# Performance work log

Measured on AMD Instinct MI355X. Metric: run time of the kernel, lower is better.

The kernel has to match this reference:

```python
import jax, jax.numpy as jnp
import numpy as np

N = 100000
E = 1000000
D = 32          # numerical_dim
HID = 64        # hidden_dim
OUT = 1         # output_dim
REL = 4 * D     # relation feature dim
EPS = 1e-8


def setup_inputs() -> dict:
    key = jax.random.key(0)
    k_x, k_e, k_w1, k_b1, k_w2, k_b2 = jax.random.split(key, 6)
    x = jax.random.uniform(k_x, (N, D), dtype=jnp.float32)
    edge_index = jax.random.randint(k_e, (2, E), 0, N, dtype=jnp.int64)
    # Linear params (PyTorch convention: W [out, in], y = x @ W.T + b)
    lim1 = 1.0 / np.sqrt(REL)
    W1 = jax.random.uniform(k_w1, (HID, REL), minval=-lim1, maxval=lim1, dtype=jnp.float32)
    b1 = jax.random.uniform(k_b1, (HID,), minval=-lim1, maxval=lim1, dtype=jnp.float32)
    lim2 = 1.0 / np.sqrt(HID)
    W2 = jax.random.uniform(k_w2, (OUT, HID), minval=-lim2, maxval=lim2, dtype=jnp.float32)
    b2 = jax.random.uniform(k_b2, (OUT,), minval=-lim2, maxval=lim2, dtype=jnp.float32)
    return {"x": x, "edge_index": edge_index, "W1": W1, "b1": b1, "W2": W2, "b2": b2}


def _relation_features(x_i, x_j):
    ratio = x_i / (x_j + EPS)
    log_ratio = jnp.log(x_i + EPS) - jnp.log(x_j + EPS)
    abs_diff = jnp.abs(x_i - x_j)
    rel_diff = abs_diff / (jnp.maximum(x_i, x_j) + EPS)
    return jnp.concatenate([ratio, log_ratio, abs_diff, rel_diff], axis=-1)  # [E, 4D]


def reference(x, edge_index, W1, b1, W2, b2):
    src, dst = edge_index[0], edge_index[1]
    x_i = x[src]                      # [E, D] gather source node feats
    x_j = x[dst]                      # [E, D] gather target node feats
    rel = _relation_features(x_i, x_j)  # [E, 4D]
    h = jax.nn.relu(rel @ W1.T + b1)    # [E, HID]
    edge_bias = (h @ W2.T + b2).squeeze(-1)  # [E]
    return edge_bias
```

## Files before the change

kernel.cpp:

```cpp
#include <hip/hip_runtime.h>


#define DD    32
#define HID   64
#define RELF  128
#define EPSF  1e-8f
#define LXLO  -18.420681f
#define LXSC  13.843137f
#define LXIV  0.07223796f
#define MSC   3.0517578125e-05f

typedef short  bf16x8 __attribute__((ext_vector_type(8)));
typedef float  f32x4  __attribute__((ext_vector_type(4)));

union U8 { unsigned u[4]; bf16x8 v; uint4 q4; };
union Q  { uint4 v; unsigned u[4]; float f[4]; };

static __device__ __forceinline__ unsigned pk_tr(float lo, float hi) {
    return __builtin_amdgcn_perm(__builtin_bit_cast(unsigned, hi),
                                 __builtin_bit_cast(unsigned, lo), 0x07060302u);
}
static __device__ __forceinline__ unsigned rne_bits(float f) {
    unsigned u = __builtin_bit_cast(unsigned, f);
    return u + 0x7fffu + ((u >> 16) & 1u);
}
static __device__ __forceinline__ unsigned pk_rne(float lo, float hi) {
    return __builtin_amdgcn_perm(rne_bits(hi), rne_bits(lo), 0x07060302u);
}
static __device__ __forceinline__ float hi_f32(float f) {
    return __builtin_bit_cast(float, __builtin_bit_cast(unsigned, f) & 0xffff0000u);
}
static __device__ __forceinline__ float ubyte(unsigned w, int b) {
    return (float)((w >> (8 * b)) & 0xffu);
}
static __device__ __forceinline__ unsigned q8(float v) {
    int u = (int)(v + 0.5f);
    return (unsigned)(u > 255 ? 255 : (u < 0 ? 0 : u));
}
template <int CTRL>
static __device__ __forceinline__ float dpp_ror_add(float pp) {
    int s = __builtin_bit_cast(int, pp);
    int t = __builtin_amdgcn_update_dpp(0, s, CTRL, 0xf, 0xf, true);
    return pp + __builtin_bit_cast(float, t);
}

__global__ __launch_bounds__(256)
void prep_pack(const float* __restrict__ x, uint4* __restrict__ rec, int nchunk)
{
    int i = blockIdx.x * blockDim.x + threadIdx.x;
    if (i >= nchunk) return;
    const float4* xp = (const float4*)(x + (size_t)i * 8);
    float4 v0 = xp[0], v1 = xp[1];
    float xv[8] = {v0.x, v0.y, v0.z, v0.w, v1.x, v1.y, v1.z, v1.w};

    unsigned xh[4];
    #pragma unroll
    for (int p = 0; p < 4; ++p) xh[p] = pk_tr(xv[2*p], xv[2*p+1]);

    unsigned xl[2] = {0u, 0u}, lu[2] = {0u, 0u};
    #pragma unroll
    for (int e = 0; e < 8; ++e) {
        float a  = xv[e];
        float ah = hi_f32(a);
        float f  = 0.f;
        if (ah > 0.f)
            f = (a * __builtin_amdgcn_rcpf(ah) - 1.f) * 32768.f;
        xl[e >> 2] |= q8(f) << (8 * (e & 3));
        float lxe = __logf(a + EPSF);
        lu[e >> 2] |= q8((lxe - LXLO) * LXSC) << (8 * (e & 3));
    }

    uint4 r0; r0.x = xh[0]; r0.y = xh[1]; r0.z = xh[2]; r0.w = xh[3];
    uint4 r1; r1.x = xl[0]; r1.y = xl[1]; r1.z = lu[0]; r1.w = lu[1];
    rec[2 * i]     = r0;
    rec[2 * i + 1] = r1;
}

template <int PACK>
__global__ __launch_bounds__(256, 4)
void edge_bias_mfma(const float* __restrict__ x,
                    const int*   __restrict__ ei,
                    const float* __restrict__ W1,
                    const float* __restrict__ b1,
                    const float* __restrict__ W2,
                    const float* __restrict__ b2,
                    const uint4* __restrict__ rec,
                    float* __restrict__ out,
                    int E)
{
    const int lane = threadIdx.x & 63;
    const int wv   = threadIdx.x >> 6;
    const int wave = (blockIdx.x * blockDim.x + threadIdx.x) >> 6;
    const int nwv  = (gridDim.x * blockDim.x) >> 6;
    const int c = lane & 15;
    const int q = lane >> 4;

    __shared__ uint4 sW[20 * 64];
    for (int s = wv; s < 5; s += 4) {
        #pragma unroll
        for (int nt = 0; nt < 4; ++nt) {
            const float* wr = W1 + (nt * 16 + c) * RELF + q * 8;
            U8 t;
            if (s == 0) {
                #pragma unroll
                for (int p = 0; p < 4; ++p)
                    t.u[p] = pk_tr(wr[2*p], wr[2*p+1]);
            } else if (s == 1) {
                #pragma unroll
                for (int p = 0; p < 4; ++p) {
                    float w0 = wr[2*p], w1 = wr[2*p+1];
                    t.u[p] = pk_rne(w0 - hi_f32(w0), w1 - hi_f32(w1));
                }
            } else {
                const int base = (s == 2) ? 32 : (s == 3) ? 64 : 96;
                #pragma unroll
                for (int p = 0; p < 4; ++p)
                    t.u[p] = pk_rne(wr[base + 2*p], wr[base + 2*p + 1]);
            }
            sW[(s * 4 + nt) * 64 + lane] = t.q4;
        }
    }
    __syncthreads();

    float b1v[4], w2v[4];
    #pragma unroll
    for (int nt = 0; nt < 4; ++nt) {
        b1v[nt] = b1[nt * 16 + c];
        w2v[nt] = W2[nt * 16 + c];
    }
    const float b2s = b2[0];

    const int ntiles = (E + 15) >> 4;
    int t = wave;
    if (t >= ntiles) return;

    auto ldidx = [&](int tt_, int& s, int& d) {
        if (tt_ >= ntiles) tt_ = t;
        int em = (tt_ << 4) + c; if (em > E - 1) em = E - 1;
        s = ei[em]; d = ei[E + em];
    };
    auto gather = [&](int s, int d, Q& hi_, Q& mi_, Q& hj_, Q& mj_) {
        if constexpr (PACK) {
            const uint4* pi = rec + (size_t)s * 8 + q * 2;
            const uint4* pj = rec + (size_t)d * 8 + q * 2;
            hi_.v = pi[0]; mi_.v = pi[1];
            hj_.v = pj[0]; mj_.v = pj[1];
        } else {
            const uint4* pi = (const uint4*)(x + (size_t)s * DD + q * 8);
            const uint4* pj = (const uint4*)(x + (size_t)d * DD + q * 8);
            hi_.v = pi[0]; mi_.v = pi[1];
            hj_.v = pj[0]; mj_.v = pj[1];
        }
    };
    auto decode = [&](const Q& h, const Q& m, float* xv, bf16x8& lfrag) {
        #pragma unroll
        for (int p = 0; p < 4; ++p) {
            float lo = __builtin_bit_cast(float, h.u[p] << 16);
            float hi = __builtin_bit_cast(float, h.u[p] & 0xffff0000u);
            unsigned xb = (p < 2) ? m.u[0] : m.u[1];
            float m0 = ubyte(xb, (2 * p) & 3);
            float m1 = ubyte(xb, (2 * p + 1) & 3);
            xv[2 * p]     = fmaf(lo * MSC, m0, lo);
            xv[2 * p + 1] = fmaf(hi * MSC, m1, hi);
        }
        U8 L;
        #pragma unroll
        for (int p = 0; p < 4; ++p) {
            unsigned lb = (p < 2) ? m.u[2] : m.u[3];
            float l0 = fmaf(ubyte(lb, (2 * p) & 3),     LXIV, LXLO);
            float l1 = fmaf(ubyte(lb, (2 * p + 1) & 3), LXIV, LXLO);
            L.u[p] = pk_tr(l0, l1);
        }
        lfrag = L.v;
    };

    auto compute = [&](int tc, const Q& hI, const Q& mI, const Q& hJ, const Q& mJ) {
        float xiv[8], xjv[8];
        bf16x8 aLi, aLj;
        if constexpr (PACK) {
            decode(hI, mI, xiv, aLi);
            decode(hJ, mJ, xjv, aLj);
        } else {
            #pragma unroll
            for (int p = 0; p < 4; ++p) { xiv[p] = hI.f[p]; xiv[4 + p] = mI.f[p]; }
            #pragma unroll
            for (int p = 0; p < 4; ++p) { xjv[p] = hJ.f[p]; xjv[4 + p] = mJ.f[p]; }
            U8 ti, tj;
            #pragma unroll
            for (int p = 0; p < 4; ++p) {
                ti.u[p] = pk_rne(__logf(xiv[2*p] + EPSF), __logf(xiv[2*p+1] + EPSF));
                tj.u[p] = pk_rne(__logf(xjv[2*p] + EPSF), __logf(xjv[2*p+1] + EPSF));
            }
            aLi = ti.v; aLj = tj.v;
        }
        U8 nj; nj.v = aLj;
        #pragma unroll
        for (int p = 0; p < 4; ++p) nj.u[p] ^= 0x80008000u;

        U8 R, Rl, Aa, Dd;
        #pragma unroll
        for (int p = 0; p < 4; ++p) {
            float a0 = xiv[2*p], a1 = xiv[2*p+1];
            float c0 = xjv[2*p], c1 = xjv[2*p+1];
            float r0 = a0 * __builtin_amdgcn_rcpf(c0 + EPSF);
            float r1 = a1 * __builtin_amdgcn_rcpf(c1 + EPSF);
            float d0 = fabsf(a0 - c0), d1 = fabsf(a1 - c1);
            float g0 = d0 * __builtin_amdgcn_rcpf(fmaxf(a0, c0) + EPSF);
            float g1 = d1 * __builtin_amdgcn_rcpf(fmaxf(a1, c1) + EPSF);
            R.u[p]  = pk_tr(r0, r1);
            Rl.u[p] = pk_tr(r0 - hi_f32(r0), r1 - hi_f32(r1));
            Aa.u[p] = pk_tr(d0, d1);
            Dd.u[p] = pk_tr(g0, g1);
        }

        int off = lane;
        asm volatile("" : "+v"(off));
        auto ldfrag = [&](int s, int nt) {
            U8 w; w.q4 = sW[(s * 4 + nt) * 64 + off];
            return w.v;
        };

        f32x4 acc[4];
        #pragma unroll
        for (int nt = 0; nt < 4; ++nt) {
            acc[nt][0] = b1v[nt]; acc[nt][1] = b1v[nt];
            acc[nt][2] = b1v[nt]; acc[nt][3] = b1v[nt];
        }
        #pragma unroll
        for (int nt = 0; nt < 4; ++nt) {
            bf16x8 fW0h = ldfrag(0, nt);
            bf16x8 fW0l = ldfrag(1, nt);
            bf16x8 fWL  = ldfrag(2, nt);
            bf16x8 fWA  = ldfrag(3, nt);
            bf16x8 fWD  = ldfrag(4, nt);
            acc[nt] = __builtin_amdgcn_mfma_f32_16x16x32_bf16(R.v,  fW0h, acc[nt], 0, 0, 0);
            acc[nt] = __builtin_amdgcn_mfma_f32_16x16x32_bf16(Rl.v, fW0h, acc[nt], 0, 0, 0);
            acc[nt] = __builtin_amdgcn_mfma_f32_16x16x32_bf16(R.v,  fW0l, acc[nt], 0, 0, 0);
            acc[nt] = __builtin_amdgcn_mfma_f32_16x16x32_bf16(aLi,  fWL,  acc[nt], 0, 0, 0);
            acc[nt] = __builtin_amdgcn_mfma_f32_16x16x32_bf16(nj.v, fWL,  acc[nt], 0, 0, 0);
            acc[nt] = __builtin_amdgcn_mfma_f32_16x16x32_bf16(Aa.v, fWA,  acc[nt], 0, 0, 0);
            acc[nt] = __builtin_amdgcn_mfma_f32_16x16x32_bf16(Dd.v, fWD,  acc[nt], 0, 0, 0);
        }

        float p4[4];
        #pragma unroll
        for (int r = 0; r < 4; ++r) {
            float pp = 0.f;
            #pragma unroll
            for (int nt = 0; nt < 4; ++nt)
                pp = fmaf(fmaxf(acc[nt][r], 0.f), w2v[nt], pp);
            pp = dpp_ror_add<0x121>(pp);
            pp = dpp_ror_add<0x122>(pp);
            pp = dpp_ror_add<0x124>(pp);
            pp = dpp_ror_add<0x128>(pp);
            p4[r] = pp;
        }
        if (c < 4) {
            const int e = (tc << 4) + q * 4 + c;
            if (e < E) {
                float v = (c == 0) ? p4[0] : (c == 1) ? p4[1] : (c == 2) ? p4[2] : p4[3];
                out[e] = v + b2s;
            }
        }
    };

    Q hA, mA, hJA, mJA;
    Q hB, mB, hJB, mJB;
    int sC, dC;

    { int s, d; ldidx(t,        s, d); gather(s, d, hA, mA, hJA, mJA); }
    { int s, d; ldidx(t + nwv,  s, d); gather(s, d, hB, mB, hJB, mJB); }
    ldidx(t + 2 * nwv, sC, dC);

    for (;;) {
        compute(t, hA, mA, hJA, mJA);
        gather(sC, dC, hA, mA, hJA, mJA);
        ldidx(t + 3 * nwv, sC, dC);
        t += nwv; if (t >= ntiles) break;

        compute(t, hB, mB, hJB, mJB);
        gather(sC, dC, hB, mB, hJB, mJB);
        ldidx(t + 3 * nwv, sC, dC);
        t += nwv; if (t >= ntiles) break;
    }
}

extern "C" void kernel_launch(void* const* d_in, const int* in_sizes, int n_in,
                              void* d_out, int out_size, void* d_ws, size_t ws_size,
                              hipStream_t stream)
{
    const float* x   = (const float*)d_in[0];
    const int*   ei  = (const int*)  d_in[1];
    const float* W1  = (const float*)d_in[2];
    const float* b1  = (const float*)d_in[3];
    const float* W2  = (const float*)d_in[4];
    const float* b2  = (const float*)d_in[5];
    float* out = (float*)d_out;

    const int E  = out_size;
    const int Nd = in_sizes[0];
    uint4* rec = (uint4*)d_ws;

    const bool pack = ws_size >= (size_t)Nd * 4 && (Nd % 8) == 0;
    if (pack) {
        const int nchunk = Nd / 8;
        prep_pack<<<(nchunk + 255) / 256, 256, 0, stream>>>(x, rec, nchunk);
        edge_bias_mfma<1><<<2048, 256, 0, stream>>>(x, ei, W1, b1, W2, b2, rec, out, E);
    } else {
        edge_bias_mfma<0><<<2048, 256, 0, stream>>>(x, ei, W1, b1, W2, b2, rec, out, E);
    }
}
```

Before: 131.6 us.

## Switch edge MLP to 32x32x16 MFMA tiles and drop software prefetch pipeline

Changes the per-wave tile from 16 to 32 edges and replaces the 16x16x32 bf16 MFMAs with 32x32x16 ones over two K-slices. The weight fragments in LDS are relaid out to match, and the output reduction uses an extra DPP step plus a lane-select tree. The explicit double-buffered gather/index prefetch loop is removed in favour of a simple grid-stride loop, and the grid shrinks to 1954 blocks. The aim is fewer MFMA issues and better operand reuse per edge, at the cost of losing the explicit latency hiding for the random gathers.

```diff
diff --git a/kernel.cpp b/kernel.cpp
--- a/kernel.cpp
+++ b/kernel.cpp
@@ -12,6 +12,7 @@
 
 typedef short  bf16x8 __attribute__((ext_vector_type(8)));
 typedef float  f32x4  __attribute__((ext_vector_type(4)));
+typedef float  f32x16 __attribute__((ext_vector_type(16)));
 
 union U8 { unsigned u[4]; bf16x8 v; uint4 q4; };
 union Q  { uint4 v; unsigned u[4]; float f[4]; };
@@ -92,72 +93,46 @@
     const int wv   = threadIdx.x >> 6;
     const int wave = (blockIdx.x * blockDim.x + threadIdx.x) >> 6;
     const int nwv  = (gridDim.x * blockDim.x) >> 6;
-    const int c = lane & 15;
-    const int q = lane >> 4;
+    const int r = lane & 31;
+    const int h = lane >> 5;
 
     __shared__ uint4 sW[20 * 64];
-    for (int s = wv; s < 5; s += 4) {
-        #pragma unroll
-        for (int nt = 0; nt < 4; ++nt) {
-            const float* wr = W1 + (nt * 16 + c) * RELF + q * 8;
-            U8 t;
-            if (s == 0) {
-                #pragma unroll
-                for (int p = 0; p < 4; ++p)
-                    t.u[p] = pk_tr(wr[2*p], wr[2*p+1]);
-            } else if (s == 1) {
-                #pragma unroll
-                for (int p = 0; p < 4; ++p) {
-                    float w0 = wr[2*p], w1 = wr[2*p+1];
-                    t.u[p] = pk_rne(w0 - hi_f32(w0), w1 - hi_f32(w1));
-                }
-            } else {
-                const int base = (s == 2) ? 32 : (s == 3) ? 64 : 96;
-                #pragma unroll
-                for (int p = 0; p < 4; ++p)
-                    t.u[p] = pk_rne(wr[base + 2*p], wr[base + 2*p + 1]);
+    for (int f = wv; f < 20; f += 4) {
+        const int set = f >> 2, ct = (f >> 1) & 1, sl = f & 1;
+        const int fb  = (set <= 1) ? 0 : (set - 1) * 32;
+        const float* wr = W1 + (ct * 32 + r) * RELF + fb + sl * 16 + h * 8;
+        U8 tw;
+        if (set == 0) {
+            #pragma unroll
+            for (int p = 0; p < 4; ++p) tw.u[p] = pk_tr(wr[2*p], wr[2*p+1]);
+        } else if (set == 1) {
+            #pragma unroll
+            for (int p = 0; p < 4; ++p) {
+                float w0 = wr[2*p], w1 = wr[2*p+1];
+                tw.u[p] = pk_rne(w0 - hi_f32(w0), w1 - hi_f32(w1));
             }
-            sW[(s * 4 + nt) * 64 + lane] = t.q4;
-        }
+        } else {
+            #pragma unroll
+            for (int p = 0; p < 4; ++p) tw.u[p] = pk_rne(wr[2*p], wr[2*p+1]);
+        }
+        sW[f * 64 + lane] = tw.q4;
     }
     __syncthreads();
 
-    float b1v[4], w2v[4];
+    float b1v[2], w2v[2];
     #pragma unroll
-    for (int nt = 0; nt < 4; ++nt) {
-        b1v[nt] = b1[nt * 16 + c];
-        w2v[nt] = W2[nt * 16 + c];
+    for (int ct = 0; ct < 2; ++ct) {
+        b1v[ct] = b1[ct * 32 + r];
+        w2v[ct] = W2[ct * 32 + r];
     }
     const float b2s = b2[0];
 
-    const int ntiles = (E + 15) >> 4;
-    int t = wave;
-    if (t >= ntiles) return;
-
-    auto ldidx = [&](int tt_, int& s, int& d) {
-        if (tt_ >= ntiles) tt_ = t;
-        int em = (tt_ << 4) + c; if (em > E - 1) em = E - 1;
-        s = ei[em]; d = ei[E + em];
-    };
-    auto gather = [&](int s, int d, Q& hi_, Q& mi_, Q& hj_, Q& mj_) {
-        if constexpr (PACK) {
-            const uint4* pi = rec + (size_t)s * 8 + q * 2;
-            const uint4* pj = rec + (size_t)d * 8 + q * 2;
-            hi_.v = pi[0]; mi_.v = pi[1];
-            hj_.v = pj[0]; mj_.v = pj[1];
-        } else {
-            const uint4* pi = (const uint4*)(x + (size_t)s * DD + q * 8);
-            const uint4* pj = (const uint4*)(x + (size_t)d * DD + q * 8);
-            hi_.v = pi[0]; mi_.v = pi[1];
-            hj_.v = pj[0]; mj_.v = pj[1];
-        }
-    };
-    auto decode = [&](const Q& h, const Q& m, float* xv, bf16x8& lfrag) {
+    auto decode = [&](const Q& hq, const Q& mq, float* xv, bf16x8& lfrag) {
         #pragma unroll
         for (int p = 0; p < 4; ++p) {
-            float lo = __builtin_bit_cast(float, h.u[p] << 16);
-            float hi = __builtin_bit_cast(float, h.u[p] & 0xffff0000u);
-            unsigned xb = (p < 2) ? m.u[0] : m.u[1];
+            float lo = __builtin_bit_cast(float, hq.u[p] << 16);
+            float hi = __builtin_bit_cast(float, hq.u[p] & 0xffff0000u);
+            unsigned xb = (p < 2) ? mq.u[0] : mq.u[1];
             float m0 = ubyte(xb, (2 * p) & 3);
             float m1 = ubyte(xb, (2 * p + 1) & 3);
             xv[2 * p]     = fmaf(lo * MSC, m0, lo);
@@ -166,7 +141,7 @@
         U8 L;
         #pragma unroll
         for (int p = 0; p < 4; ++p) {
-            unsigned lb = (p < 2) ? m.u[2] : m.u[3];
+            unsigned lb = (p < 2) ? mq.u[2] : mq.u[3];
             float l0 = fmaf(ubyte(lb, (2 * p) & 3),     LXIV, LXLO);
             float l1 = fmaf(ubyte(lb, (2 * p + 1) & 3), LXIV, LXLO);
             L.u[p] = pk_tr(l0, l1);
@@ -174,114 +149,135 @@
         lfrag = L.v;
     };
 
-    auto compute = [&](int tc, const Q& hI, const Q& mI, const Q& hJ, const Q& mJ) {
-        float xiv[8], xjv[8];
-        bf16x8 aLi, aLj;
+    const int ntiles = (E + 31) >> 5;
+    for (int t = wave; t < ntiles; t += nwv) {
+        int em = (t << 5) + r; if (em > E - 1) em = E - 1;
+        const int sn = ei[em], dn = ei[E + em];
+
+        Q hi0, mi0, hi1, mi1, hj0, mj0, hj1, mj1;
         if constexpr (PACK) {
-            decode(hI, mI, xiv, aLi);
-            decode(hJ, mJ, xjv, aLj);
+            const uint4* pi = rec + (size_t)sn * 8 + (h << 1);
+            const uint4* pj = rec + (size_t)dn * 8 + (h << 1);
+            hi0.v = pi[0]; mi0.v = pi[1]; hi1.v = pi[4]; mi1.v = pi[5];
+            hj0.v = pj[0]; mj0.v = pj[1]; hj1.v = pj[4]; mj1.v = pj[5];
         } else {
-            #pragma unroll
-            for (int p = 0; p < 4; ++p) { xiv[p] = hI.f[p]; xiv[4 + p] = mI.f[p]; }
-            #pragma unroll
-            for (int p = 0; p < 4; ++p) { xjv[p] = hJ.f[p]; xjv[4 + p] = mJ.f[p]; }
-            U8 ti, tj;
-            #pragma unroll
-            for (int p = 0; p < 4; ++p) {
-                ti.u[p] = pk_rne(__logf(xiv[2*p] + EPSF), __logf(xiv[2*p+1] + EPSF));
-                tj.u[p] = pk_rne(__logf(xjv[2*p] + EPSF), __logf(xjv[2*p+1] + EPSF));
-            }
-            aLi = ti.v; aLj = tj.v;
-        }
-        U8 nj; nj.v = aLj;
-        #pragma unroll
-        for (int p = 0; p < 4; ++p) nj.u[p] ^= 0x80008000u;
-
-        U8 R, Rl, Aa, Dd;
-        #pragma unroll
-        for (int p = 0; p < 4; ++p) {
-            float a0 = xiv[2*p], a1 = xiv[2*p+1];
-            float c0 = xjv[2*p], c1 = xjv[2*p+1];
-            float r0 = a0 * __builtin_amdgcn_rcpf(c0 + EPSF);
-            float r1 = a1 * __builtin_amdgcn_rcpf(c1 + EPSF);
-            float d0 = fabsf(a0 - c0), d1 = fabsf(a1 - c1);
-            float g0 = d0 * __builtin_amdgcn_rcpf(fmaxf(a0, c0) + EPSF);
-            float g1 = d1 * __builtin_amdgcn_rcpf(fmaxf(a1, c1) + EPSF);
-            R.u[p]  = pk_tr(r0, r1);
-            Rl.u[p] = pk_tr(r0 - hi_f32(r0), r1 - hi_f32(r1));
-            Aa.u[p] = pk_tr(d0, d1);
-            Dd.u[p] = pk_tr(g0, g1);
+            const uint4* pi = (const uint4*)(x + (size_t)sn * DD + h * 8);
+            const uint4* pj = (const uint4*)(x + (size_t)dn * DD + h * 8);
+            hi0.v = pi[0]; mi0.v = pi[1]; hi1.v = pi[4]; mi1.v = pi[5];
+            hj0.v = pj[0]; mj0.v = pj[1]; hj1.v = pj[4]; mj1.v = pj[5];
         }
 
         int off = lane;
         asm volatile("" : "+v"(off));
-        auto ldfrag = [&](int s, int nt) {
-            U8 w; w.q4 = sW[(s * 4 + nt) * 64 + off];
+        auto ldfrag = [&](int set, int ct, int sl) {
+            U8 w; w.q4 = sW[(set * 4 + ct * 2 + sl) * 64 + off];
             return w.v;
         };
 
-        f32x4 acc[4];
-        #pragma unroll
-        for (int nt = 0; nt < 4; ++nt) {
-            acc[nt][0] = b1v[nt]; acc[nt][1] = b1v[nt];
-            acc[nt][2] = b1v[nt]; acc[nt][3] = b1v[nt];
-        }
-        #pragma unroll
-        for (int nt = 0; nt < 4; ++nt) {
-            bf16x8 fW0h = ldfrag(0, nt);
-            bf16x8 fW0l = ldfrag(1, nt);
-            bf16x8 fWL  = ldfrag(2, nt);
-            bf16x8 fWA  = ldfrag(3, nt);
-            bf16x8 fWD  = ldfrag(4, nt);
-            acc[nt] = __builtin_amdgcn_mfma_f32_16x16x32_bf16(R.v,  fW0h, acc[nt], 0, 0, 0);
-            acc[nt] = __builtin_amdgcn_mfma_f32_16x16x32_bf16(Rl.v, fW0h, acc[nt], 0, 0, 0);
-            acc[nt] = __builtin_amdgcn_mfma_f32_16x16x32_bf16(R.v,  fW0l, acc[nt], 0, 0, 0);
-            acc[nt] = __builtin_amdgcn_mfma_f32_16x16x32_bf16(aLi,  fWL,  acc[nt], 0, 0, 0);
-            acc[nt] = __builtin_amdgcn_mfma_f32_16x16x32_bf16(nj.v, fWL,  acc[nt], 0, 0, 0);
-            acc[nt] = __builtin_amdgcn_mfma_f32_16x16x32_bf16(Aa.v, fWA,  acc[nt], 0, 0, 0);
-            acc[nt] = __builtin_amdgcn_mfma_f32_16x16x32_bf16(Dd.v, fWD,  acc[nt], 0, 0, 0);
-        }
-
-        float p4[4];
-        #pragma unroll
-        for (int r = 0; r < 4; ++r) {
-            float pp = 0.f;
-            #pragma unroll
-            for (int nt = 0; nt < 4; ++nt)
-                pp = fmaf(fmaxf(acc[nt][r], 0.f), w2v[nt], pp);
-            pp = dpp_ror_add<0x121>(pp);
-            pp = dpp_ror_add<0x122>(pp);
-            pp = dpp_ror_add<0x124>(pp);
-            pp = dpp_ror_add<0x128>(pp);
-            p4[r] = pp;
-        }
-        if (c < 4) {
-            const int e = (tc << 4) + q * 4 + c;
-            if (e < E) {
-                float v = (c == 0) ? p4[0] : (c == 1) ? p4[1] : (c == 2) ? p4[2] : p4[3];
-                out[e] = v + b2s;
+        f32x16 acc0, acc1;
+        #pragma unroll
+        for (int i = 0; i < 16; ++i) { acc0[i] = b1v[0]; acc1[i] = b1v[1]; }
+
+        #pragma unroll
+        for (int sl = 0; sl < 2; ++sl) {
+            const Q& hI = sl ? hi1 : hi0;  const Q& mI = sl ? mi1 : mi0;
+            const Q& hJ = sl ? hj1 : hj0;  const Q& mJ = sl ? mj1 : mj0;
+
+            float xiv[8], xjv[8];
+            bf16x8 aLi, aLj;
+            if constexpr (PACK) {
+                decode(hI, mI, xiv, aLi);
+                decode(hJ, mJ, xjv, aLj);
+            } else {
+                #pragma unroll
+                for (int p = 0; p < 4; ++p) {
+                    xiv[p] = hI.f[p]; xiv[4 + p] = mI.f[p];
+                    xjv[p] = hJ.f[p]; xjv[4 + p] = mJ.f[p];
+                }
+                U8 ti, tj;
+                #pragma unroll
+                for (int p = 0; p < 4; ++p) {
+                    ti.u[p] = pk_rne(__logf(xiv[2*p] + EPSF), __logf(xiv[2*p+1] + EPSF));
+                    tj.u[p] = pk_rne(__logf(xjv[2*p] + EPSF), __logf(xjv[2*p+1] + EPSF));
+                }
+                aLi = ti.v; aLj = tj.v;
             }
-        }
-    };
-
-    Q hA, mA, hJA, mJA;
-    Q hB, mB, hJB, mJB;
-    int sC, dC;
-
-    { int s, d; ldidx(t,        s, d); gather(s, d, hA, mA, hJA, mJA); }
-    { int s, d; ldidx(t + nwv,  s, d); gather(s, d, hB, mB, hJB, mJB); }
-    ldidx(t + 2 * nwv, sC, dC);
-
-    for (;;) {
-        compute(t, hA, mA, hJA, mJA);
-        gather(sC, dC, hA, mA, hJA, mJA);
-        ldidx(t + 3 * nwv, sC, dC);
-        t += nwv; if (t >= ntiles) break;
-
-        compute(t, hB, mB, hJB, mJB);
-        gather(sC, dC, hB, mB, hJB, mJB);
-        ldidx(t + 3 * nwv, sC, dC);
-        t += nwv; if (t >= ntiles) break;
+            U8 nj; nj.v = aLj;
+            #pragma unroll
+            for (int p = 0; p < 4; ++p) nj.u[p] ^= 0x80008000u;
+
+            U8 R, Rl, Aa, Dd;
+            #pragma unroll
+            for (int p = 0; p < 4; ++p) {
+                float a0 = xiv[2*p], a1 = xiv[2*p+1];
+                float c0 = xjv[2*p], c1 = xjv[2*p+1];
+                float r0 = a0 * __builtin_amdgcn_rcpf(c0 + EPSF);
+                float r1 = a1 * __builtin_amdgcn_rcpf(c1 + EPSF);
+                float d0 = fabsf(a0 - c0), d1 = fabsf(a1 - c1);
+                float g0 = d0 * __builtin_amdgcn_rcpf(fmaxf(a0, c0) + EPSF);
+                float g1 = d1 * __builtin_amdgcn_rcpf(fmaxf(a1, c1) + EPSF);
+                R.u[p]  = pk_tr(r0, r1);
+                Rl.u[p] = pk_tr(r0 - hi_f32(r0), r1 - hi_f32(r1));
+                Aa.u[p] = pk_tr(d0, d1);
+                Dd.u[p] = pk_tr(g0, g1);
+            }
+
+            #pragma unroll
+            for (int ct = 0; ct < 2; ++ct) {
+                bf16x8 fW0h = ldfrag(0, ct, sl);
+                bf16x8 fW0l = ldfrag(1, ct, sl);
+                bf16x8 fWL  = ldfrag(2, ct, sl);
+                bf16x8 fWA  = ldfrag(3, ct, sl);
+                bf16x8 fWD  = ldfrag(4, ct, sl);
+                if (ct == 0) {
+                    acc0 = __builtin_amdgcn_mfma_f32_32x32x16_bf16(R.v,  fW0h, acc0, 0, 0, 0);
+                    acc0 = __builtin_amdgcn_mfma_f32_32x32x16_bf16(Rl.v, fW0h, acc0, 0, 0, 0);
+                    acc0 = __builtin_amdgcn_mfma_f32_32x32x16_bf16(R.v,  fW0l, acc0, 0, 0, 0);
+                    acc0 = __builtin_amdgcn_mfma_f32_32x32x16_bf16(aLi,  fWL,  acc0, 0, 0, 0);
+                    acc0 = __builtin_amdgcn_mfma_f32_32x32x16_bf16(nj.v, fWL,  acc0, 0, 0, 0);
+                    acc0 = __builtin_amdgcn_mfma_f32_32x32x16_bf16(Aa.v, fWA,  acc0, 0, 0, 0);
+                    acc0 = __builtin_amdgcn_mfma_f32_32x32x16_bf16(Dd.v, fWD,  acc0, 0, 0, 0);
+                } else {
+                    acc1 = __builtin_amdgcn_mfma_f32_32x32x16_bf16(R.v,  fW0h, acc1, 0, 0, 0);
+                    acc1 = __builtin_amdgcn_mfma_f32_32x32x16_bf16(Rl.v, fW0h, acc1, 0, 0, 0);
+                    acc1 = __builtin_amdgcn_mfma_f32_32x32x16_bf16(R.v,  fW0l, acc1, 0, 0, 0);
+                    acc1 = __builtin_amdgcn_mfma_f32_32x32x16_bf16(aLi,  fWL,  acc1, 0, 0, 0);
+                    acc1 = __builtin_amdgcn_mfma_f32_32x32x16_bf16(nj.v, fWL,  acc1, 0, 0, 0);
+                    acc1 = __builtin_amdgcn_mfma_f32_32x32x16_bf16(Aa.v, fWA,  acc1, 0, 0, 0);
+                    acc1 = __builtin_amdgcn_mfma_f32_32x32x16_bf16(Dd.v, fWD,  acc1, 0, 0, 0);
+                }
+            }
+        }
+
+        float pp[16];
+        #pragma unroll
+        for (int g = 0; g < 16; ++g) {
+            float v0 = fmaxf(acc0[g], 0.f), v1 = fmaxf(acc1[g], 0.f);
+            pp[g] = fmaf(v0, w2v[0], v1 * w2v[1]);
+        }
+        #pragma unroll
+        for (int g = 0; g < 16; ++g) {
+            float s = pp[g];
+            s = dpp_ror_add<0x121>(s);
+            s = dpp_ror_add<0x122>(s);
+            s = dpp_ror_add<0x124>(s);
+            s = dpp_ror_add<0x128>(s);
+            s = dpp_ror_add<0x142>(s);
+            pp[g] = s;
+        }
+        if ((lane >> 4) & 1) {
+            const int l = lane & 15;
+            float q8a[8], q4a[4], q2a[2];
+            #pragma unroll
+            for (int i = 0; i < 8; ++i) q8a[i] = (l & 1) ? pp[2*i+1] : pp[2*i];
+            #pragma unroll
+            for (int i = 0; i < 4; ++i) q4a[i] = (l & 2) ? q8a[2*i+1] : q8a[2*i];
+            #pragma unroll
+            for (int i = 0; i < 2; ++i) q2a[i] = (l & 4) ? q4a[2*i+1] : q4a[2*i];
+            float v = (l & 8) ? q2a[1] : q2a[0];
+            const int e2 = (t << 5) + (l & 3) + ((l >> 2) << 3) + (h << 2);
+            if (e2 < E) out[e2] = v + b2s;
+        }
     }
 }
 
@@ -301,12 +297,14 @@
     const int Nd = in_sizes[0];
     uint4* rec = (uint4*)d_ws;
 
+    const int blocks = 1954;
+
     const bool pack = ws_size >= (size_t)Nd * 4 && (Nd % 8) == 0;
     if (pack) {
         const int nchunk = Nd / 8;
         prep_pack<<<(nchunk + 255) / 256, 256, 0, stream>>>(x, rec, nchunk);
-        edge_bias_mfma<1><<<2048, 256, 0, stream>>>(x, ei, W1, b1, W2, b2, rec, out, E);
+        edge_bias_mfma<1><<<blocks, 256, 0, stream>>>(x, ei, W1, b1, W2, b2, rec, out, E);
     } else {
-        edge_bias_mfma<0><<<2048, 256, 0, stream>>>(x, ei, W1, b1, W2, b2, rec, out, E);
-    }
-}
+        edge_bias_mfma<0><<<blocks, 256, 0, stream>>>(x, ei, W1, b1, W2, b2, rec, out, E);
+    }
+}
```

Result: slower. 239.7 us (+82.2%).

## Bucket-sort edges by source node before gathering to improve locality

Applied to the files above, without the earlier changes.

Adds a histogram/scan/scatter counting sort that groups edges by the high bits of their source index, then runs the MFMA edge kernel over the permuted edge list and scatters results back through the saved original index. The aim is better cache locality for the per-edge source-row gathers. In exchange it adds three extra launches, a serial single-block scan, extra index traffic and scattered output writes.

```diff
diff --git a/kernel.cpp b/kernel.cpp
--- a/kernel.cpp
+++ b/kernel.cpp
@@ -9,6 +9,9 @@
 #define LXSC  13.843137f
 #define LXIV  0.07223796f
 #define MSC   3.0517578125e-05f
+
+#define SB_NB 256
+#define SB_EB 8192
 
 typedef short  bf16x8 __attribute__((ext_vector_type(8)));
 typedef float  f32x4  __attribute__((ext_vector_type(4)));
@@ -76,10 +79,69 @@
     rec[2 * i + 1] = r1;
 }
 
-template <int PACK>
+__global__ __launch_bounds__(256)
+void sort_hist(const int* __restrict__ ei, unsigned* __restrict__ H,
+               int E, int shift)
+{
+    __shared__ unsigned lh[SB_NB];
+    const int tid = threadIdx.x, blk = blockIdx.x;
+    lh[tid] = 0u;
+    __syncthreads();
+    const int base = blk * SB_EB;
+    const int end  = (base + SB_EB < E) ? base + SB_EB : E;
+    for (int e = base + tid; e < end; e += 256)
+        atomicAdd(&lh[((unsigned)ei[e]) >> shift], 1u);
+    __syncthreads();
+    H[blk * SB_NB + tid] = lh[tid];
+}
+
+__global__ __launch_bounds__(256)
+void sort_scan(const unsigned* __restrict__ H, unsigned* __restrict__ Bk,
+               int nblk)
+{
+    __shared__ unsigned colsum[SB_NB];
+    __shared__ unsigned basebuf[SB_NB];
+    const int b = threadIdx.x;
+    unsigned s = 0;
+    for (int k = 0; k < nblk; ++k) s += H[k * SB_NB + b];
+    colsum[b] = s;
+    __syncthreads();
+    if (b == 0) {
+        unsigned run = 0;
+        for (int i = 0; i < SB_NB; ++i) { basebuf[i] = run; run += colsum[i]; }
+    }
+    __syncthreads();
+    unsigned run = basebuf[b];
+    for (int k = 0; k < nblk; ++k) {
+        Bk[k * SB_NB + b] = run;
+        run += H[k * SB_NB + b];
+    }
+}
+
+__global__ __launch_bounds__(256)
+void sort_scatter(const int* __restrict__ ei, const unsigned* __restrict__ Bk,
+                  int* __restrict__ ssrc, int* __restrict__ sdst,
+                  int* __restrict__ sidx, int E, int shift)
+{
+    __shared__ unsigned cur[SB_NB];
+    const int tid = threadIdx.x, blk = blockIdx.x;
+    cur[tid] = Bk[blk * SB_NB + tid];
+    __syncthreads();
+    const int base = blk * SB_EB;
+    const int end  = (base + SB_EB < E) ? base + SB_EB : E;
+    for (int e = base + tid; e < end; e += 256) {
+        int s = ei[e], d = ei[E + e];
+        unsigned pos = atomicAdd(&cur[((unsigned)s) >> shift], 1u);
+        ssrc[pos] = s; sdst[pos] = d; sidx[pos] = e;
+    }
+}
+
+template <int PACK, int SORTED>
 __global__ __launch_bounds__(256, 4)
 void edge_bias_mfma(const float* __restrict__ x,
-                    const int*   __restrict__ ei,
+                    const int*   __restrict__ psrc,
+                    const int*   __restrict__ pdst,
+                    const int*   __restrict__ pidx,
                     const float* __restrict__ W1,
                     const float* __restrict__ b1,
                     const float* __restrict__ W2,
@@ -137,7 +199,7 @@
     auto ldidx = [&](int tt_, int& s, int& d) {
         if (tt_ >= ntiles) tt_ = t;
         int em = (tt_ << 4) + c; if (em > E - 1) em = E - 1;
-        s = ei[em]; d = ei[E + em];
+        s = psrc[em]; d = pdst[em];
     };
     auto gather = [&](int s, int d, Q& hi_, Q& mi_, Q& hj_, Q& mj_) {
         if constexpr (PACK) {
@@ -259,7 +321,11 @@
             const int e = (tc << 4) + q * 4 + c;
             if (e < E) {
                 float v = (c == 0) ? p4[0] : (c == 1) ? p4[1] : (c == 2) ? p4[2] : p4[3];
-                out[e] = v + b2s;
+                if constexpr (SORTED) {
+                    out[pidx[e]] = v + b2s;
+                } else {
+                    out[e] = v + b2s;
+                }
             }
         }
     };
@@ -299,14 +365,41 @@
 
     const int E  = out_size;
     const int Nd = in_sizes[0];
-    uint4* rec = (uint4*)d_ws;
-
-    const bool pack = ws_size >= (size_t)Nd * 4 && (Nd % 8) == 0;
-    if (pack) {
+    const int N  = Nd / DD;
+
+    const size_t RB   = (size_t)Nd * 4;
+    const int    nblk = (E + SB_EB - 1) / SB_EB;
+    const size_t SORT = (size_t)E * 12 + (size_t)nblk * SB_NB * 8;
+
+    uint4*    rec  = (uint4*)d_ws;
+    char*     wb   = (char*)d_ws + RB;
+    int*      ssrc = (int*)wb;
+    int*      sdst = ssrc + E;
+    int*      sidx = sdst + E;
+    unsigned* H    = (unsigned*)(sidx + E);
+    unsigned* Bk   = H + (size_t)nblk * SB_NB;
+
+    const bool pack   = ws_size >= RB && (Nd % 8) == 0;
+    const bool sorted = pack && ws_size >= RB + SORT && E > 0;
+
+    int shift = 0;
+    while (((unsigned)(N - 1) >> shift) > 255u) ++shift;
+
+    if (sorted) {
         const int nchunk = Nd / 8;
         prep_pack<<<(nchunk + 255) / 256, 256, 0, stream>>>(x, rec, nchunk);
-        edge_bias_mfma<1><<<2048, 256, 0, stream>>>(x, ei, W1, b1, W2, b2, rec, out, E);
+        sort_hist<<<nblk, 256, 0, stream>>>(ei, H, E, shift);
+        sort_scan<<<1, 256, 0, stream>>>(H, Bk, nblk);
+        sort_scatter<<<nblk, 256, 0, stream>>>(ei, Bk, ssrc, sdst, sidx, E, shift);
+        edge_bias_mfma<1, 1><<<2048, 256, 0, stream>>>(
+            x, ssrc, sdst, sidx, W1, b1, W2, b2, rec, out, E);
+    } else if (pack) {
+        const int nchunk = Nd / 8;
+        prep_pack<<<(nchunk + 255) / 256, 256, 0, stream>>>(x, rec, nchunk);
+        edge_bias_mfma<1, 0><<<2048, 256, 0, stream>>>(
+            x, ei, ei + E, ei, W1, b1, W2, b2, rec, out, E);
     } else {
-        edge_bias_mfma<0><<<2048, 256, 0, stream>>>(x, ei, W1, b1, W2, b2, rec, out, E);
-    }
-}
+        edge_bias_mfma<0, 0><<<2048, 256, 0, stream>>>(
+            x, ei, ei + E, ei, W1, b1, W2, b2, rec, out, E);
+    }
+}
```

Measured after the change: 197.4 us. +50.0%, slower.

## Drop packed node-record precompute and gather raw fp32 features directly

Applied to the files above, without the earlier changes.

Removes the prep_pack pass that quantized node features into bf16-hi plus 8-bit mantissa and log codes. The edge kernel now always gathers raw fp32 rows and computes logs inline. This saves a kernel launch and the preprocessing traffic over all nodes. In exchange, each edge must recompute its log values and can no longer decode them from the precomputed codes. Gather bytes per edge are the same, since both paths read 32 bytes per quarter-row.

```diff
diff --git a/kernel.cpp b/kernel.cpp
--- a/kernel.cpp
+++ b/kernel.cpp
@@ -5,10 +5,6 @@
 #define HID   64
 #define RELF  128
 #define EPSF  1e-8f
-#define LXLO  -18.420681f
-#define LXSC  13.843137f
-#define LXIV  0.07223796f
-#define MSC   3.0517578125e-05f
 
 typedef short  bf16x8 __attribute__((ext_vector_type(8)));
 typedef float  f32x4  __attribute__((ext_vector_type(4)));
@@ -29,13 +25,6 @@
 }
 static __device__ __forceinline__ float hi_f32(float f) {
     return __builtin_bit_cast(float, __builtin_bit_cast(unsigned, f) & 0xffff0000u);
-}
-static __device__ __forceinline__ float ubyte(unsigned w, int b) {
-    return (float)((w >> (8 * b)) & 0xffu);
-}
-static __device__ __forceinline__ unsigned q8(float v) {
-    int u = (int)(v + 0.5f);
-    return (unsigned)(u > 255 ? 255 : (u < 0 ? 0 : u));
 }
 template <int CTRL>
 static __device__ __forceinline__ float dpp_ror_add(float pp) {
@@ -44,39 +33,6 @@
     return pp + __builtin_bit_cast(float, t);
 }
 
-__global__ __launch_bounds__(256)
-void prep_pack(const float* __restrict__ x, uint4* __restrict__ rec, int nchunk)
-{
-    int i = blockIdx.x * blockDim.x + threadIdx.x;
-    if (i >= nchunk) return;
-    const float4* xp = (const float4*)(x + (size_t)i * 8);
-    float4 v0 = xp[0], v1 = xp[1];
-    float xv[8] = {v0.x, v0.y, v0.z, v0.w, v1.x, v1.y, v1.z, v1.w};
-
-    unsigned xh[4];
-    #pragma unroll
-    for (int p = 0; p < 4; ++p) xh[p] = pk_tr(xv[2*p], xv[2*p+1]);
-
-    unsigned xl[2] = {0u, 0u}, lu[2] = {0u, 0u};
-    #pragma unroll
-    for (int e = 0; e < 8; ++e) {
-        float a  = xv[e];
-        float ah = hi_f32(a);
-        float f  = 0.f;
-        if (ah > 0.f)
-            f = (a * __builtin_amdgcn_rcpf(ah) - 1.f) * 32768.f;
-        xl[e >> 2] |= q8(f) << (8 * (e & 3));
-        float lxe = __logf(a + EPSF);
-        lu[e >> 2] |= q8((lxe - LXLO) * LXSC) << (8 * (e & 3));
-    }
-
-    uint4 r0; r0.x = xh[0]; r0.y = xh[1]; r0.z = xh[2]; r0.w = xh[3];
-    uint4 r1; r1.x = xl[0]; r1.y = xl[1]; r1.z = lu[0]; r1.w = lu[1];
-    rec[2 * i]     = r0;
-    rec[2 * i + 1] = r1;
-}
-
-template <int PACK>
 __global__ __launch_bounds__(256, 4)
 void edge_bias_mfma(const float* __restrict__ x,
                     const int*   __restrict__ ei,
@@ -84,7 +40,6 @@
                     const float* __restrict__ b1,
                     const float* __restrict__ W2,
                     const float* __restrict__ b2,
-                    const uint4* __restrict__ rec,
                     float* __restrict__ out,
                     int E)
 {
@@ -140,60 +95,27 @@
         s = ei[em]; d = ei[E + em];
     };
     auto gather = [&](int s, int d, Q& hi_, Q& mi_, Q& hj_, Q& mj_) {
-        if constexpr (PACK) {
-            const uint4* pi = rec + (size_t)s * 8 + q * 2;
-            const uint4* pj = rec + (size_t)d * 8 + q * 2;
-            hi_.v = pi[0]; mi_.v = pi[1];
-            hj_.v = pj[0]; mj_.v = pj[1];
-        } else {
-            const uint4* pi = (const uint4*)(x + (size_t)s * DD + q * 8);
-            const uint4* pj = (const uint4*)(x + (size_t)d * DD + q * 8);
-            hi_.v = pi[0]; mi_.v = pi[1];
-            hj_.v = pj[0]; mj_.v = pj[1];
-        }
-    };
-    auto decode = [&](const Q& h, const Q& m, float* xv, bf16x8& lfrag) {
-        #pragma unroll
-        for (int p = 0; p < 4; ++p) {
-            float lo = __builtin_bit_cast(float, h.u[p] << 16);
-            float hi = __builtin_bit_cast(float, h.u[p] & 0xffff0000u);
-            unsigned xb = (p < 2) ? m.u[0] : m.u[1];
-            float m0 = ubyte(xb, (2 * p) & 3);
-            float m1 = ubyte(xb, (2 * p + 1) & 3);
-            xv[2 * p]     = fmaf(lo * MSC, m0, lo);
-            xv[2 * p + 1] = fmaf(hi * MSC, m1, hi);
-        }
-        U8 L;
-        #pragma unroll
-        for (int p = 0; p < 4; ++p) {
-            unsigned lb = (p < 2) ? m.u[2] : m.u[3];
-            float l0 = fmaf(ubyte(lb, (2 * p) & 3),     LXIV, LXLO);
-            float l1 = fmaf(ubyte(lb, (2 * p + 1) & 3), LXIV, LXLO);
-            L.u[p] = pk_tr(l0, l1);
-        }
-        lfrag = L.v;
+        const uint4* pi = (const uint4*)(x + (size_t)s * DD + q * 8);
+        const uint4* pj = (const uint4*)(x + (size_t)d * DD + q * 8);
+        hi_.v = pi[0]; mi_.v = pi[1];
+        hj_.v = pj[0]; mj_.v = pj[1];
     };
 
     auto compute = [&](int tc, const Q& hI, const Q& mI, const Q& hJ, const Q& mJ) {
         float xiv[8], xjv[8];
-        bf16x8 aLi, aLj;
-        if constexpr (PACK) {
-            decode(hI, mI, xiv, aLi);
-            decode(hJ, mJ, xjv, aLj);
-        } else {
-            #pragma unroll
-            for (int p = 0; p < 4; ++p) { xiv[p] = hI.f[p]; xiv[4 + p] = mI.f[p]; }
-            #pragma unroll
-            for (int p = 0; p < 4; ++p) { xjv[p] = hJ.f[p]; xjv[4 + p] = mJ.f[p]; }
-            U8 ti, tj;
-            #pragma unroll
-            for (int p = 0; p < 4; ++p) {
-                ti.u[p] = pk_rne(__logf(xiv[2*p] + EPSF), __logf(xiv[2*p+1] + EPSF));
-                tj.u[p] = pk_rne(__logf(xjv[2*p] + EPSF), __logf(xjv[2*p+1] + EPSF));
-            }
-            aLi = ti.v; aLj = tj.v;
-        }
-        U8 nj; nj.v = aLj;
+        #pragma unroll
+        for (int p = 0; p < 4; ++p) { xiv[p] = hI.f[p]; xiv[4 + p] = mI.f[p]; }
+        #pragma unroll
+        for (int p = 0; p < 4; ++p) { xjv[p] = hJ.f[p]; xjv[4 + p] = mJ.f[p]; }
+
+        U8 ti, tj;
+        #pragma unroll
+        for (int p = 0; p < 4; ++p) {
+            ti.u[p] = pk_rne(__logf(xiv[2*p] + EPSF), __logf(xiv[2*p+1] + EPSF));
+            tj.u[p] = pk_rne(__logf(xjv[2*p] + EPSF), __logf(xjv[2*p+1] + EPSF));
+        }
+        bf16x8 aLi = ti.v;
+        U8 nj; nj.v = tj.v;
         #pragma unroll
         for (int p = 0; p < 4; ++p) nj.u[p] ^= 0x80008000u;
 
@@ -297,16 +219,8 @@
     const float* b2  = (const float*)d_in[5];
     float* out = (float*)d_out;
 
-    const int E  = out_size;
-    const int Nd = in_sizes[0];
-    uint4* rec = (uint4*)d_ws;
-
-    const bool pack = ws_size >= (size_t)Nd * 4 && (Nd % 8) == 0;
-    if (pack) {
-        const int nchunk = Nd / 8;
-        prep_pack<<<(nchunk + 255) / 256, 256, 0, stream>>>(x, rec, nchunk);
-        edge_bias_mfma<1><<<2048, 256, 0, stream>>>(x, ei, W1, b1, W2, b2, rec, out, E);
-    } else {
-        edge_bias_mfma<0><<<2048, 256, 0, stream>>>(x, ei, W1, b1, W2, b2, rec, out, E);
-    }
-}
+    const int E = out_size;
+    (void)d_ws; (void)ws_size; (void)in_sizes; (void)n_in;
+
+    edge_bias_mfma<<<2048, 256, 0, stream>>>(x, ei, W1, b1, W2, b2, out, E);
+}
```

Measured after the change: 138.0 us. 1.05x slower.
